# Performance work log

Measured on AMD Instinct MI355X. Metric: run time of the kernel, lower is better.

The kernel has to match this reference:

```python
import jax, jax.numpy as jnp
import numpy as np

B, T, C, H = 2, 2048, 768, 12
D = C // H              # head_dim = 64
LOCAL_WINDOW = 256
LN_EPS = 1e-5


def _layernorm(x, w, b):
    mu = jnp.mean(x, axis=-1, keepdims=True)
    var = jnp.var(x, axis=-1, keepdims=True)
    return (x - mu) * jax.lax.rsqrt(var + LN_EPS) * w + b


def setup_inputs() -> dict:
    key = jax.random.key(0)
    ks = jax.random.split(key, 8)
    inp = {
        "x": jax.random.normal(ks[0], (B, T, C), dtype=jnp.float32),
        "mamba_raw": jax.random.normal(ks[1], (B, T, C), dtype=jnp.float32),
        # c_attn / c_proj per nn.init in __init__
        "c_attn_w": 0.02 * jax.random.normal(ks[2], (C, 3 * C), dtype=jnp.float32),
        "c_attn_b": jnp.zeros((3 * C,), dtype=jnp.float32),
        "c_proj_w": 0.02 * jax.random.normal(ks[3], (C, C), dtype=jnp.float32),
        "c_proj_b": jnp.zeros((C,), dtype=jnp.float32),
        "ln_w": jnp.ones((C,), dtype=jnp.float32),
        "ln_b": jnp.zeros((C,), dtype=jnp.float32),
        "mamba_scale": jnp.asarray(0.1, dtype=jnp.float32),
        "sel_w": 0.01 * jax.random.normal(ks[4], (C, 1), dtype=jnp.float32),
        "sel_b": jnp.zeros((1,), dtype=jnp.float32),
        "local_weight": jnp.asarray(0.5, dtype=jnp.float32),
        "global_weight": jnp.asarray(0.5, dtype=jnp.float32),
    }
    return inp


def reference(x, mamba_raw, c_attn_w, c_attn_b, c_proj_w, c_proj_b,
              ln_w, ln_b, mamba_scale, sel_w, sel_b, local_weight, global_weight):
    scale = D ** -0.5
    qkv = x @ c_attn_w + c_attn_b                       # (B,T,3C)
    q, k, v = jnp.split(qkv, 3, axis=-1)
    q = q.reshape(B, T, H, D)
    k = k.reshape(B, T, H, D)
    v = v.reshape(B, T, H, D)

    scores = jnp.einsum('bihd,bjhd->bhij', q, k) * scale  # (B,H,T,T)
    i = jnp.arange(T)[:, None]
    j = jnp.arange(T)[None, :]
    causal = j > i                                       # mask strictly-future keys
    neg_inf = jnp.asarray(-jnp.inf, dtype=scores.dtype)
    scores = jnp.where(causal, neg_inf, scores)

    # frozen mamba branch (mamba_raw is a constant activation)
    mamba_raw = jax.lax.stop_gradient(mamba_raw)
    mamba_scaled = mamba_scale * _layernorm(mamba_raw, ln_w, ln_b)   # (B,T,C)
    sel = jax.nn.sigmoid(mamba_scaled @ sel_w + sel_b)               # (B,T,1)
    sel = sel[:, None, :, 0][:, :, None, :]                          # (B,1,1,T) over keys

    attn_global = scores * (0.5 + 0.5 * sel)             # -inf stays -inf

    outside_local = j < jnp.maximum(i - LOCAL_WINDOW, 0)
    attn_local = jnp.where(outside_local, neg_inf, scores)

    w_l = jax.nn.sigmoid(local_weight)
    w_g = jax.nn.sigmoid(global_weight)
    w_sum = w_l + w_g
    w_l, w_g = w_l / w_sum, w_g / w_sum

    attn_combined = w_l * jax.nn.softmax(attn_local, axis=-1) \
                  + w_g * jax.nn.softmax(attn_global, axis=-1)

    out = jnp.einsum('bhij,bjhd->bihd', attn_combined, v).reshape(B, T, C)
    return out @ c_proj_w + c_proj_b
```

## Files before the change

kernel.cpp:

```cpp
#include <hip/hip_runtime.h>
#include <math.h>

#define Bsz 2
#define Tsz 2048
#define Csz 768
#define Hsz 12
#define C3  2304
#define WIN 256
#define LN_EPS 1e-5f

#define QSCALE 0.1803368801111137f

typedef short bf16x8 __attribute__((ext_vector_type(8)));
typedef float f32x4  __attribute__((ext_vector_type(4)));

__device__ __forceinline__ unsigned short f2b(float f) {
    unsigned int u = __float_as_uint(f);
    u = (u + 0x7fffu + ((u >> 16) & 1u)) >> 16;
    return (unsigned short)u;
}

__device__ __forceinline__ float fast_exp2(float x) {
    float r;
    asm("v_exp_f32 %0, %1" : "=v"(r) : "v"(x));
    return r;
}

__global__ __launch_bounds__(256) void prep_fused(
    const float* __restrict__ x, unsigned short* __restrict__ xb,
    const float* __restrict__ c_attn_w, unsigned short* __restrict__ wq,
    const float* __restrict__ c_proj_w, unsigned short* __restrict__ wp,
    const float* __restrict__ mr, const float* __restrict__ ln_w,
    const float* __restrict__ ln_b, const float* __restrict__ scale_p,
    const float* __restrict__ sel_w, const float* __restrict__ sel_b,
    float* __restrict__ sel)
{
    __shared__ float tile[32][33];
    __shared__ float red1[256];
    __shared__ float red2[256];
    __shared__ float mu_sh, rstd_sh;

    const int blk = blockIdx.x;
    const int tid = threadIdx.x;

    if (blk < 3072) {
        int idx = blk * 256 + tid;
        float4 v = *(const float4*)(x + (size_t)idx * 4);
        unsigned int lo = (unsigned int)f2b(v.x) | ((unsigned int)f2b(v.y) << 16);
        unsigned int hi = (unsigned int)f2b(v.z) | ((unsigned int)f2b(v.w) << 16);
        uint2 o; o.x = lo; o.y = hi;
        *(uint2*)(xb + (size_t)idx * 4) = o;
        return;
    }
    if (blk < 5376) {
        const float* src; unsigned short* dst; int K, N, n0, k0;
        if (blk < 4800) {
            int i = blk - 3072;
            src = c_attn_w; dst = wq; K = Csz; N = C3;
            n0 = (i % 72) * 32; k0 = (i / 72) * 32;
        } else {
            int i = blk - 4800;
            src = c_proj_w; dst = wp; K = Csz; N = Csz;
            n0 = (i % 24) * 32; k0 = (i / 24) * 32;
        }
        const int tx = tid & 31, ty = tid >> 5;
        #pragma unroll
        for (int p = 0; p < 4; ++p)
            tile[ty + p * 8][tx] = src[(size_t)(k0 + ty + p * 8) * N + n0 + tx];
        __syncthreads();
        #pragma unroll
        for (int p = 0; p < 4; ++p)
            dst[(size_t)(n0 + ty + p * 8) * K + k0 + tx] = f2b(tile[tx][ty + p * 8]);
        return;
    }

    const int r = blk - 5376;
    const float* row = mr + (size_t)r * Csz;

    float s = 0.f, s2 = 0.f;
    for (int c = tid; c < Csz; c += 256) {
        float xv = row[c];
        s += xv; s2 += xv * xv;
    }
    red1[tid] = s; red2[tid] = s2;
    __syncthreads();
    for (int st = 128; st > 0; st >>= 1) {
        if (tid < st) { red1[tid] += red1[tid + st]; red2[tid] += red2[tid + st]; }
        __syncthreads();
    }
    if (tid == 0) {
        float mu = red1[0] * (1.f / Csz);
        float var = red2[0] * (1.f / Csz) - mu * mu;
        mu_sh = mu;
        rstd_sh = rsqrtf(var + LN_EPS);
    }
    __syncthreads();
    const float mu = mu_sh, rstd = rstd_sh;

    float dot = 0.f;
    for (int c = tid; c < Csz; c += 256) {
        float xn = (row[c] - mu) * rstd * ln_w[c] + ln_b[c];
        dot += xn * sel_w[c];
    }
    red1[tid] = dot;
    __syncthreads();
    for (int st = 128; st > 0; st >>= 1) {
        if (tid < st) red1[tid] += red1[tid + st];
        __syncthreads();
    }
    if (tid == 0) {
        float z = scale_p[0] * red1[0] + sel_b[0];
        sel[r] = 0.5f + 0.5f / (1.f + __expf(-z));
    }
}

__global__ __launch_bounds__(256) void pack_fused(
    const unsigned short* __restrict__ qkv, unsigned short* __restrict__ KP,
    unsigned short* __restrict__ VP)
{
    __shared__ unsigned short tile[32][72];

    if (blockIdx.x < 1536) {
        const int g = blockIdx.x * 4 + (threadIdx.x >> 6);
        const int lane = threadIdx.x & 63;
        const int lm = lane & 15, quad = lane >> 4;
        const int f = g & 1;
        const int kt = (g >> 1) & 127;
        const int bh = g >> 8;
        const int b = bh / Hsz, h = bh % Hsz;
        const unsigned short* src = qkv +
            (size_t)(b * Tsz + kt * 16 + lm) * C3 + Csz + h * 64 + f * 32 + quad * 8;
        bf16x8 v = *(const bf16x8*)src;
        *(bf16x8*)(KP + (size_t)g * 512 + lane * 8) = v;
        return;
    }

    const int g = blockIdx.x - 1536;
    const int jt = g & 63;
    const int bh = g >> 6;
    const int b = bh / Hsz, h = bh % Hsz;

    const int row = threadIdx.x >> 3, dc = (threadIdx.x & 7) * 8;
    *(bf16x8*)&tile[row][dc] = *(const bf16x8*)(
        qkv + (size_t)(b * Tsz + jt * 32 + row) * C3 + 2 * Csz + h * 64 + dc);
    __syncthreads();

    const int lane = threadIdx.x & 63, nt = threadIdx.x >> 6;
    const int lm = lane & 15, quad = lane >> 4;
    unsigned short tmp[8];
    #pragma unroll
    for (int j = 0; j < 8; ++j) tmp[j] = tile[quad * 8 + j][nt * 16 + lm];
    *(bf16x8*)(VP + ((size_t)(bh * 64 + jt) * 4 + nt) * 512 + lane * 8) =
        *(bf16x8*)tmp;
}

template<int OUT_BF16>
__global__ __launch_bounds__(256) void gemm_bt_mfma(
    const unsigned short* __restrict__ A, const unsigned short* __restrict__ BT,
    const float* __restrict__ bias, void* __restrict__ Cout,
    int M, int N, int K, int scale_cols)
{
    __shared__ unsigned short As[128 * 32];
    __shared__ unsigned short Bs[128 * 32];

    const int tid = threadIdx.x;
    const int lane = tid & 63, widx = tid >> 6;
    const int lm = lane & 15, quad = lane >> 4;
    const int wm = widx >> 1, wn = widx & 1;
    const int m0 = blockIdx.y * 128, n0 = blockIdx.x * 128;

    f32x4 acc[4][4];
    #pragma unroll
    for (int mt = 0; mt < 4; ++mt)
        #pragma unroll
        for (int nt = 0; nt < 4; ++nt)
            acc[mt][nt] = f32x4{0.f, 0.f, 0.f, 0.f};

    int rowS[2], cS[2];
    #pragma unroll
    for (int t = 0; t < 2; ++t) {
        int idx = t * 256 + tid;
        rowS[t] = idx >> 2;
        cS[t] = idx & 3;
    }

    bf16x8 pa[2], pb[2];
    #pragma unroll
    for (int t = 0; t < 2; ++t) {
        pa[t] = *(const bf16x8*)(A + (size_t)(m0 + rowS[t]) * K + cS[t] * 8);
        pb[t] = *(const bf16x8*)(BT + (size_t)(n0 + rowS[t]) * K + cS[t] * 8);
    }

    const int nk = K / 32;
    for (int kt = 0; kt < nk; ++kt) {
        __syncthreads();
        #pragma unroll
        for (int t = 0; t < 2; ++t) {
            *(bf16x8*)(&As[rowS[t] * 32 + ((cS[t] ^ ((rowS[t] >> 1) & 3)) << 3)]) = pa[t];
            *(bf16x8*)(&Bs[rowS[t] * 32 + ((cS[t] ^ ((rowS[t] >> 1) & 3)) << 3)]) = pb[t];
        }
        __syncthreads();
        if (kt + 1 < nk) {
            int k0 = (kt + 1) * 32;
            #pragma unroll
            for (int t = 0; t < 2; ++t) {
                pa[t] = *(const bf16x8*)(A + (size_t)(m0 + rowS[t]) * K + k0 + cS[t] * 8);
                pb[t] = *(const bf16x8*)(BT + (size_t)(n0 + rowS[t]) * K + k0 + cS[t] * 8);
            }
        }
        bf16x8 af[4], bf[4];
        #pragma unroll
        for (int mt = 0; mt < 4; ++mt) {
            int m = wm * 64 + mt * 16 + lm;
            af[mt] = *(const bf16x8*)(&As[m * 32 + ((quad ^ ((m >> 1) & 3)) << 3)]);
        }
        #pragma unroll
        for (int nt = 0; nt < 4; ++nt) {
            int n = wn * 64 + nt * 16 + lm;
            bf[nt] = *(const bf16x8*)(&Bs[n * 32 + ((quad ^ ((n >> 1) & 3)) << 3)]);
        }
        #pragma unroll
        for (int mt = 0; mt < 4; ++mt)
            #pragma unroll
            for (int nt = 0; nt < 4; ++nt)
                acc[mt][nt] = __builtin_amdgcn_mfma_f32_16x16x32_bf16(
                    af[mt], bf[nt], acc[mt][nt], 0, 0, 0);
    }

    float bv[4], scl[4];
    #pragma unroll
    for (int nt = 0; nt < 4; ++nt) {
        bv[nt] = bias[n0 + wn * 64 + nt * 16 + lm];
        scl[nt] = ((n0 + wn * 64 + nt * 16) < scale_cols) ? QSCALE : 1.0f;
    }

    #pragma unroll
    for (int mt = 0; mt < 4; ++mt) {
        #pragma unroll
        for (int nt = 0; nt < 4; ++nt) {
            int col = n0 + wn * 64 + nt * 16 + lm;
            #pragma unroll
            for (int r = 0; r < 4; ++r) {
                int row = m0 + wm * 64 + mt * 16 + quad * 4 + r;
                float v = (acc[mt][nt][r] + bv[nt]) * scl[nt];
                if (OUT_BF16)
                    ((unsigned short*)Cout)[(size_t)row * N + col] = f2b(v);
                else
                    ((float*)Cout)[(size_t)row * N + col] = v;
            }
        }
    }
}

__global__ __launch_bounds__(256) void attn_mfma(
    const unsigned short* __restrict__ qkv, const unsigned short* __restrict__ KP,
    const unsigned short* __restrict__ VP, const float* __restrict__ fsel_arr,
    const float* __restrict__ lw_p, const float* __restrict__ gw_p,
    unsigned short* __restrict__ attnb)
{
    __shared__ __align__(16) unsigned char SMEM[18432];

    const int tid = threadIdx.x;
    const int widx = tid >> 6, lane = tid & 63;
    const int lm = lane & 15, quad = lane >> 4;

    unsigned short* Pg = (unsigned short*)SMEM + (widx * 2 + 0) * (16 * 72);
    unsigned short* Pl = (unsigned short*)SMEM + (widx * 2 + 1) * (16 * 72);
    float* MrgF = (float*)SMEM;
    #define MRG(slot, br, row, col) MrgF[((((slot) * 2 + (br)) * 16 + (row)) * 66) + (col)]

    const int strip = 127 - (int)(blockIdx.x / 24);
    const int bh = (int)(blockIdx.x % 24);
    const int h = bh % Hsz, b = bh / Hsz;
    const int i0 = strip * 16;

    const unsigned short* qkv_b = qkv + (size_t)b * Tsz * C3;
    const unsigned short* KPb = KP + (size_t)bh * 131072 + lane * 8;
    const unsigned short* VPb = VP + (size_t)bh * 131072 + lane * 8;

    const unsigned short* qrow = qkv_b + (size_t)(i0 + lm) * C3 + h * 64 + quad * 8;
    const bf16x8 qf0 = *(const bf16x8*)qrow;
    const bf16x8 qf1 = *(const bf16x8*)(qrow + 32);

    float l_g[4], l_l[4];
    f32x4 Og[4], Ol[4];
    #pragma unroll
    for (int r = 0; r < 4; ++r) { l_g[r] = 0.f; l_l[r] = 0.f; }
    #pragma unroll
    for (int nt = 0; nt < 4; ++nt) {
        Og[nt] = f32x4{0.f, 0.f, 0.f, 0.f};
        Ol[nt] = f32x4{0.f, 0.f, 0.f, 0.f};
    }

    const int jtd = i0 >> 6;
    const int jtl = (jtd - 4) > 0 ? (jtd - 4) : 0;

    for (int jt = widx; jt <= jtd; jt += 4) {
        const int j0 = jt * 64;
        const bool diag = (jt == jtd);
        const bool firstloc = (jt == jtl) && !diag;
        const bool loc = (jt >= jtl);

        const unsigned short* kp = KPb + (size_t)(j0 >> 4) * 1024;
        bf16x8 kc0[4], kc1[4];
        #pragma unroll
        for (int nt = 0; nt < 4; ++nt) {
            kc0[nt] = *(const bf16x8*)(kp + nt * 1024);
            kc1[nt] = *(const bf16x8*)(kp + nt * 1024 + 512);
        }

        f32x4 s[4];
        #pragma unroll
        for (int nt = 0; nt < 4; ++nt) {
            f32x4 z = f32x4{0.f, 0.f, 0.f, 0.f};
            z = __builtin_amdgcn_mfma_f32_16x16x32_bf16(qf0, kc0[nt], z, 0, 0, 0);
            z = __builtin_amdgcn_mfma_f32_16x16x32_bf16(qf1, kc1[nt], z, 0, 0, 0);
            s[nt] = z;
        }

        float fs[4];
        #pragma unroll
        for (int nt = 0; nt < 4; ++nt)
            fs[nt] = fsel_arr[b * Tsz + j0 + nt * 16 + lm];

        if (diag) {
            #pragma unroll
            for (int r = 0; r < 4; ++r) {
                const int qi = i0 + quad * 4 + r;
                #pragma unroll
                for (int nt = 0; nt < 4; ++nt) {
                    const int kj = j0 + nt * 16 + lm;
                    float p = fast_exp2(s[nt][r] * fs[nt]);
                    p = (kj > qi) ? 0.f : p;
                    unsigned int u = __float_as_uint(p);
                    l_g[r] += __uint_as_float(u & 0xffff0000u);
                    Pg[(quad * 4 + r) * 72 + nt * 16 + lm] = (unsigned short)(u >> 16);
                }
            }
        } else {
            #pragma unroll
            for (int r = 0; r < 4; ++r)
                #pragma unroll
                for (int nt = 0; nt < 4; ++nt) {
                    float p = fast_exp2(s[nt][r] * fs[nt]);
                    unsigned int u = __float_as_uint(p);
                    l_g[r] += __uint_as_float(u & 0xffff0000u);
                    Pg[(quad * 4 + r) * 72 + nt * 16 + lm] = (unsigned short)(u >> 16);
                }
        }

        if (loc) {
            if (diag) {
                #pragma unroll
                for (int r = 0; r < 4; ++r) {
                    const int qi = i0 + quad * 4 + r;
                    #pragma unroll
                    for (int nt = 0; nt < 4; ++nt) {
                        const int kj = j0 + nt * 16 + lm;
                        float p = fast_exp2(s[nt][r]);
                        p = (kj > qi || kj < qi - WIN) ? 0.f : p;
                        unsigned int u = __float_as_uint(p);
                        l_l[r] += __uint_as_float(u & 0xffff0000u);
                        Pl[(quad * 4 + r) * 72 + nt * 16 + lm] = (unsigned short)(u >> 16);
                    }
                }
            } else if (firstloc) {
                #pragma unroll
                for (int r = 0; r < 4; ++r) {
                    const int qi = i0 + quad * 4 + r;
                    #pragma unroll
                    for (int nt = 0; nt < 4; ++nt) {
                        const int kj = j0 + nt * 16 + lm;
                        float p = fast_exp2(s[nt][r]);
                        p = (kj < qi - WIN) ? 0.f : p;
                        unsigned int u = __float_as_uint(p);
                        l_l[r] += __uint_as_float(u & 0xffff0000u);
                        Pl[(quad * 4 + r) * 72 + nt * 16 + lm] = (unsigned short)(u >> 16);
                    }
                }
            } else {
                #pragma unroll
                for (int r = 0; r < 4; ++r)
                    #pragma unroll
                    for (int nt = 0; nt < 4; ++nt) {
                        float p = fast_exp2(s[nt][r]);
                        unsigned int u = __float_as_uint(p);
                        l_l[r] += __uint_as_float(u & 0xffff0000u);
                        Pl[(quad * 4 + r) * 72 + nt * 16 + lm] = (unsigned short)(u >> 16);
                    }
            }
        }

        const bf16x8 ag0 = *(const bf16x8*)(&Pg[lm * 72 + quad * 8]);
        const bf16x8 ag1 = *(const bf16x8*)(&Pg[lm * 72 + 32 + quad * 8]);
        bf16x8 al0 = {}, al1 = {};
        if (loc) {
            al0 = *(const bf16x8*)(&Pl[lm * 72 + quad * 8]);
            al1 = *(const bf16x8*)(&Pl[lm * 72 + 32 + quad * 8]);
        }

        const unsigned short* vp = VPb + (size_t)(j0 >> 5) * 2048;
        #pragma unroll
        for (int nt = 0; nt < 4; ++nt) {
            bf16x8 v0 = *(const bf16x8*)(vp + nt * 512);
            bf16x8 v1 = *(const bf16x8*)(vp + 2048 + nt * 512);
            Og[nt] = __builtin_amdgcn_mfma_f32_16x16x32_bf16(ag0, v0, Og[nt], 0, 0, 0);
            Og[nt] = __builtin_amdgcn_mfma_f32_16x16x32_bf16(ag1, v1, Og[nt], 0, 0, 0);
            if (loc) {
                Ol[nt] = __builtin_amdgcn_mfma_f32_16x16x32_bf16(al0, v0, Ol[nt], 0, 0, 0);
                Ol[nt] = __builtin_amdgcn_mfma_f32_16x16x32_bf16(al1, v1, Ol[nt], 0, 0, 0);
            }
        }
    }

    #pragma unroll
    for (int st = 1; st < 16; st <<= 1) {
        #pragma unroll
        for (int r = 0; r < 4; ++r) {
            l_g[r] += __shfl_xor(l_g[r], st);
            l_l[r] += __shfl_xor(l_l[r], st);
        }
    }

    auto write_slot = [&](int slot) {
        #pragma unroll
        for (int r = 0; r < 4; ++r) {
            const int row = quad * 4 + r;
            #pragma unroll
            for (int nt = 0; nt < 4; ++nt) {
                MRG(slot, 0, row, nt * 16 + lm) = Og[nt][r];
                MRG(slot, 1, row, nt * 16 + lm) = Ol[nt][r];
            }
            if (lm == 0) {
                MRG(slot, 0, row, 65) = l_g[r];
                MRG(slot, 1, row, 65) = l_l[r];
            }
        }
    };
    auto combine_slot = [&](int slot) {
        #pragma unroll
        for (int r = 0; r < 4; ++r) {
            const int row = quad * 4 + r;
            {
                l_g[r] += MRG(slot, 0, row, 65);
                #pragma unroll
                for (int nt = 0; nt < 4; ++nt)
                    Og[nt][r] += MRG(slot, 0, row, nt * 16 + lm);
            }
            {
                l_l[r] += MRG(slot, 1, row, 65);
                #pragma unroll
                for (int nt = 0; nt < 4; ++nt)
                    Ol[nt][r] += MRG(slot, 1, row, nt * 16 + lm);
            }
        }
    };

    __syncthreads();
    if (widx == 1) write_slot(0);
    if (widx == 3) write_slot(1);
    __syncthreads();
    if (widx == 0) combine_slot(0);
    if (widx == 2) combine_slot(1);
    __syncthreads();
    if (widx == 2) write_slot(0);
    __syncthreads();

    if (widx == 0) {
        combine_slot(0);

        float wl = 1.f / (1.f + __expf(-lw_p[0]));
        float wg = 1.f / (1.f + __expf(-gw_p[0]));
        float ws = wl + wg;
        wl /= ws; wg /= ws;

        #pragma unroll
        for (int r = 0; r < 4; ++r) {
            const int row = quad * 4 + r;
            const float cg = wg / l_g[r];
            const float cl = wl / l_l[r];
            #pragma unroll
            for (int nt = 0; nt < 4; ++nt) {
                float v = Og[nt][r] * cg + Ol[nt][r] * cl;
                attnb[(size_t)(b * Tsz + i0 + row) * Csz + h * 64 + nt * 16 + lm] =
                    f2b(v);
            }
        }
    }
    #undef MRG
}

extern "C" void kernel_launch(void* const* d_in, const int* in_sizes, int n_in,
                              void* d_out, int out_size, void* d_ws, size_t ws_size,
                              hipStream_t stream)
{
    const float* x          = (const float*)d_in[0];
    const float* mamba_raw  = (const float*)d_in[1];
    const float* c_attn_w   = (const float*)d_in[2];
    const float* c_attn_b   = (const float*)d_in[3];
    const float* c_proj_w   = (const float*)d_in[4];
    const float* c_proj_b   = (const float*)d_in[5];
    const float* ln_w       = (const float*)d_in[6];
    const float* ln_b       = (const float*)d_in[7];
    const float* mamba_sc   = (const float*)d_in[8];
    const float* sel_w      = (const float*)d_in[9];
    const float* sel_b      = (const float*)d_in[10];
    const float* local_w    = (const float*)d_in[11];
    const float* global_w   = (const float*)d_in[12];
    float* out = (float*)d_out;

    const int M = Bsz * Tsz;

    unsigned short* xb    = (unsigned short*)d_ws;
    unsigned short* wq    = xb + (size_t)M * Csz;
    unsigned short* wp    = wq + (size_t)C3 * Csz;
    unsigned short* qkvb  = wp + (size_t)Csz * Csz;
    unsigned short* kpb   = qkvb + (size_t)M * C3;
    unsigned short* vpb   = kpb + (size_t)24 * 131072;
    unsigned short* attnb = vpb + (size_t)24 * 131072;
    float* sel = (float*)(attnb + (size_t)M * Csz);

    prep_fused<<<9472, 256, 0, stream>>>(x, xb, c_attn_w, wq, c_proj_w, wp,
                                         mamba_raw, ln_w, ln_b, mamba_sc,
                                         sel_w, sel_b, sel);

    {
        dim3 g(C3 / 128, M / 128);
        gemm_bt_mfma<1><<<g, 256, 0, stream>>>(xb, wq, c_attn_b, qkvb,
                                               M, C3, Csz, Csz);
    }

    pack_fused<<<3072, 256, 0, stream>>>(qkvb, kpb, vpb);

    attn_mfma<<<128 * Hsz * Bsz, 256, 0, stream>>>(qkvb, kpb, vpb, sel,
                                                   local_w, global_w, attnb);

    {
        dim3 g(Csz / 128, M / 128);
        gemm_bt_mfma<0><<<g, 256, 0, stream>>>(attnb, wp, c_proj_b, out,
                                               M, Csz, Csz, 0);
    }
}
```

Measured before the change: 198.0 us.

## Fuse K/V packing into QKV GEMM epilogue and double-buffer attention tiles

The QKV projection GEMM now writes Q to a compact buffer and scatters K and V straight into the MFMA-friendly packed layouts, so the separate pack kernel and the full qkv intermediate are gone. The attention loop processes two key tiles per iteration: it runs the score and softmax phase for both before their PV phases, using doubled shared memory for the P buffers to expose more independent work. The trade-offs are scattered 2-byte global stores in the GEMM epilogue and twice the LDS per block, which may lower occupancy.

New measurement: 193.9 us. 2.1% less time.

```diff
diff --git a/kernel.cpp b/kernel.cpp
--- a/kernel.cpp
+++ b/kernel.cpp
@@ -114,51 +114,12 @@
     }
 }
 
-__global__ __launch_bounds__(256) void pack_fused(
-    const unsigned short* __restrict__ qkv, unsigned short* __restrict__ KP,
-    unsigned short* __restrict__ VP)
-{
-    __shared__ unsigned short tile[32][72];
-
-    if (blockIdx.x < 1536) {
-        const int g = blockIdx.x * 4 + (threadIdx.x >> 6);
-        const int lane = threadIdx.x & 63;
-        const int lm = lane & 15, quad = lane >> 4;
-        const int f = g & 1;
-        const int kt = (g >> 1) & 127;
-        const int bh = g >> 8;
-        const int b = bh / Hsz, h = bh % Hsz;
-        const unsigned short* src = qkv +
-            (size_t)(b * Tsz + kt * 16 + lm) * C3 + Csz + h * 64 + f * 32 + quad * 8;
-        bf16x8 v = *(const bf16x8*)src;
-        *(bf16x8*)(KP + (size_t)g * 512 + lane * 8) = v;
-        return;
-    }
-
-    const int g = blockIdx.x - 1536;
-    const int jt = g & 63;
-    const int bh = g >> 6;
-    const int b = bh / Hsz, h = bh % Hsz;
-
-    const int row = threadIdx.x >> 3, dc = (threadIdx.x & 7) * 8;
-    *(bf16x8*)&tile[row][dc] = *(const bf16x8*)(
-        qkv + (size_t)(b * Tsz + jt * 32 + row) * C3 + 2 * Csz + h * 64 + dc);
-    __syncthreads();
-
-    const int lane = threadIdx.x & 63, nt = threadIdx.x >> 6;
-    const int lm = lane & 15, quad = lane >> 4;
-    unsigned short tmp[8];
-    #pragma unroll
-    for (int j = 0; j < 8; ++j) tmp[j] = tile[quad * 8 + j][nt * 16 + lm];
-    *(bf16x8*)(VP + ((size_t)(bh * 64 + jt) * 4 + nt) * 512 + lane * 8) =
-        *(bf16x8*)tmp;
-}
-
-template<int OUT_BF16>
+template<int MODE>
 __global__ __launch_bounds__(256) void gemm_bt_mfma(
     const unsigned short* __restrict__ A, const unsigned short* __restrict__ BT,
     const float* __restrict__ bias, void* __restrict__ Cout,
-    int M, int N, int K, int scale_cols)
+    unsigned short* __restrict__ KP, unsigned short* __restrict__ VP,
+    int M, int N, int K)
 {
     __shared__ unsigned short As[128 * 32];
     __shared__ unsigned short Bs[128 * 32];
@@ -227,45 +188,72 @@
                     af[mt], bf[nt], acc[mt][nt], 0, 0, 0);
     }
 
-    float bv[4], scl[4];
-    #pragma unroll
-    for (int nt = 0; nt < 4; ++nt) {
+    float bv[4];
+    #pragma unroll
+    for (int nt = 0; nt < 4; ++nt)
         bv[nt] = bias[n0 + wn * 64 + nt * 16 + lm];
-        scl[nt] = ((n0 + wn * 64 + nt * 16) < scale_cols) ? QSCALE : 1.0f;
-    }
 
     #pragma unroll
     for (int mt = 0; mt < 4; ++mt) {
         #pragma unroll
         for (int nt = 0; nt < 4; ++nt) {
-            int col = n0 + wn * 64 + nt * 16 + lm;
-            #pragma unroll
-            for (int r = 0; r < 4; ++r) {
-                int row = m0 + wm * 64 + mt * 16 + quad * 4 + r;
-                float v = (acc[mt][nt][r] + bv[nt]) * scl[nt];
-                if (OUT_BF16)
-                    ((unsigned short*)Cout)[(size_t)row * N + col] = f2b(v);
-                else
-                    ((float*)Cout)[(size_t)row * N + col] = v;
+            const int cb = n0 + wn * 64 + nt * 16;
+            const int col = cb + lm;
+            const int rbase = m0 + wm * 64 + mt * 16 + quad * 4;
+            if (MODE == 0) {
+                #pragma unroll
+                for (int r = 0; r < 4; ++r)
+                    ((float*)Cout)[(size_t)(rbase + r) * N + col] =
+                        acc[mt][nt][r] + bv[nt];
+            } else if (cb < Csz) {
+                #pragma unroll
+                for (int r = 0; r < 4; ++r)
+                    ((unsigned short*)Cout)[(size_t)(rbase + r) * Csz + col] =
+                        f2b((acc[mt][nt][r] + bv[nt]) * QSCALE);
+            } else if (cb < 2 * Csz) {
+                const int dfull = col - Csz;
+                const int h = dfull >> 6, dd = dfull & 63;
+                const int f = dd >> 5, qd = (dd >> 3) & 3, j = dd & 7;
+                #pragma unroll
+                for (int r = 0; r < 4; ++r) {
+                    const int row = rbase + r;
+                    const int b = row >> 11, t = row & 2047;
+                    const int ktk = t >> 4, lmk = t & 15;
+                    size_t addr = ((((size_t)((b * Hsz + h) * 128 + ktk)) * 2 + f) * 512)
+                                  + (qd * 16 + lmk) * 8 + j;
+                    KP[addr] = f2b(acc[mt][nt][r] + bv[nt]);
+                }
+            } else {
+                const int dfull = col - 2 * Csz;
+                const int h = dfull >> 6, dd = dfull & 63;
+                const int ntv = dd >> 4, lmv = dd & 15;
+                #pragma unroll
+                for (int r = 0; r < 4; ++r) {
+                    const int row = rbase + r;
+                    const int b = row >> 11, t = row & 2047;
+                    const int jtv = t >> 5, qv = (t >> 3) & 3, j = t & 7;
+                    size_t addr = (((size_t)((b * Hsz + h) * 64 + jtv) * 4 + ntv) * 512)
+                                  + (qv * 16 + lmv) * 8 + j;
+                    VP[addr] = f2b(acc[mt][nt][r] + bv[nt]);
+                }
             }
         }
     }
 }
 
 __global__ __launch_bounds__(256) void attn_mfma(
-    const unsigned short* __restrict__ qkv, const unsigned short* __restrict__ KP,
+    const unsigned short* __restrict__ qb, const unsigned short* __restrict__ KP,
     const unsigned short* __restrict__ VP, const float* __restrict__ fsel_arr,
     const float* __restrict__ lw_p, const float* __restrict__ gw_p,
     unsigned short* __restrict__ attnb)
 {
-    __shared__ __align__(16) unsigned char SMEM[18432];
+    __shared__ __align__(16) unsigned char SMEM[36864];
 
     const int tid = threadIdx.x;
     const int widx = tid >> 6, lane = tid & 63;
     const int lm = lane & 15, quad = lane >> 4;
 
-    unsigned short* Pg = (unsigned short*)SMEM + (widx * 2 + 0) * (16 * 72);
-    unsigned short* Pl = (unsigned short*)SMEM + (widx * 2 + 1) * (16 * 72);
+    unsigned short* Pb = (unsigned short*)SMEM + widx * 4 * (16 * 72);
     float* MrgF = (float*)SMEM;
     #define MRG(slot, br, row, col) MrgF[((((slot) * 2 + (br)) * 16 + (row)) * 66) + (col)]
 
@@ -274,11 +262,11 @@
     const int h = bh % Hsz, b = bh / Hsz;
     const int i0 = strip * 16;
 
-    const unsigned short* qkv_b = qkv + (size_t)b * Tsz * C3;
     const unsigned short* KPb = KP + (size_t)bh * 131072 + lane * 8;
     const unsigned short* VPb = VP + (size_t)bh * 131072 + lane * 8;
 
-    const unsigned short* qrow = qkv_b + (size_t)(i0 + lm) * C3 + h * 64 + quad * 8;
+    const unsigned short* qrow =
+        qb + (size_t)(b * Tsz + i0 + lm) * Csz + h * 64 + quad * 8;
     const bf16x8 qf0 = *(const bf16x8*)qrow;
     const bf16x8 qf1 = *(const bf16x8*)(qrow + 32);
 
@@ -295,26 +283,23 @@
     const int jtd = i0 >> 6;
     const int jtl = (jtd - 4) > 0 ? (jtd - 4) : 0;
 
-    for (int jt = widx; jt <= jtd; jt += 4) {
+    auto phaseA = [&](int jt, int slot) {
         const int j0 = jt * 64;
         const bool diag = (jt == jtd);
         const bool firstloc = (jt == jtl) && !diag;
         const bool loc = (jt >= jtl);
+        unsigned short* Pg = Pb + (slot * 2 + 0) * (16 * 72);
+        unsigned short* Pl = Pb + (slot * 2 + 1) * (16 * 72);
 
         const unsigned short* kp = KPb + (size_t)(j0 >> 4) * 1024;
-        bf16x8 kc0[4], kc1[4];
+        f32x4 s[4];
         #pragma unroll
         for (int nt = 0; nt < 4; ++nt) {
-            kc0[nt] = *(const bf16x8*)(kp + nt * 1024);
-            kc1[nt] = *(const bf16x8*)(kp + nt * 1024 + 512);
-        }
-
-        f32x4 s[4];
-        #pragma unroll
-        for (int nt = 0; nt < 4; ++nt) {
+            bf16x8 k0 = *(const bf16x8*)(kp + nt * 1024);
+            bf16x8 k1 = *(const bf16x8*)(kp + nt * 1024 + 512);
             f32x4 z = f32x4{0.f, 0.f, 0.f, 0.f};
-            z = __builtin_amdgcn_mfma_f32_16x16x32_bf16(qf0, kc0[nt], z, 0, 0, 0);
-            z = __builtin_amdgcn_mfma_f32_16x16x32_bf16(qf1, kc1[nt], z, 0, 0, 0);
+            z = __builtin_amdgcn_mfma_f32_16x16x32_bf16(qf0, k0, z, 0, 0, 0);
+            z = __builtin_amdgcn_mfma_f32_16x16x32_bf16(qf1, k1, z, 0, 0, 0);
             s[nt] = z;
         }
 
@@ -390,6 +375,13 @@
                     }
             }
         }
+    };
+
+    auto phaseB = [&](int jt, int slot) {
+        const int j0 = jt * 64;
+        const bool loc = (jt >= jtl);
+        unsigned short* Pg = Pb + (slot * 2 + 0) * (16 * 72);
+        unsigned short* Pl = Pb + (slot * 2 + 1) * (16 * 72);
 
         const bf16x8 ag0 = *(const bf16x8*)(&Pg[lm * 72 + quad * 8]);
         const bf16x8 ag1 = *(const bf16x8*)(&Pg[lm * 72 + 32 + quad * 8]);
@@ -411,6 +403,15 @@
                 Ol[nt] = __builtin_amdgcn_mfma_f32_16x16x32_bf16(al1, v1, Ol[nt], 0, 0, 0);
             }
         }
+    };
+
+    for (int jt = widx; jt <= jtd; jt += 8) {
+        const int jt2 = jt + 4;
+        const bool has2 = (jt2 <= jtd);
+        phaseA(jt, 0);
+        if (has2) phaseA(jt2, 1);
+        phaseB(jt, 0);
+        if (has2) phaseB(jt2, 1);
     }
 
     #pragma unroll
@@ -514,8 +515,8 @@
     unsigned short* xb    = (unsigned short*)d_ws;
     unsigned short* wq    = xb + (size_t)M * Csz;
     unsigned short* wp    = wq + (size_t)C3 * Csz;
-    unsigned short* qkvb  = wp + (size_t)Csz * Csz;
-    unsigned short* kpb   = qkvb + (size_t)M * C3;
+    unsigned short* qb    = wp + (size_t)Csz * Csz;
+    unsigned short* kpb   = qb + (size_t)M * Csz;
     unsigned short* vpb   = kpb + (size_t)24 * 131072;
     unsigned short* attnb = vpb + (size_t)24 * 131072;
     float* sel = (float*)(attnb + (size_t)M * Csz);
@@ -526,18 +527,16 @@
 
     {
         dim3 g(C3 / 128, M / 128);
-        gemm_bt_mfma<1><<<g, 256, 0, stream>>>(xb, wq, c_attn_b, qkvb,
-                                               M, C3, Csz, Csz);
-    }
-
-    pack_fused<<<3072, 256, 0, stream>>>(qkvb, kpb, vpb);
-
-    attn_mfma<<<128 * Hsz * Bsz, 256, 0, stream>>>(qkvb, kpb, vpb, sel,
+        gemm_bt_mfma<1><<<g, 256, 0, stream>>>(xb, wq, c_attn_b, qb,
+                                               kpb, vpb, M, C3, Csz);
+    }
+
+    attn_mfma<<<128 * Hsz * Bsz, 256, 0, stream>>>(qb, kpb, vpb, sel,
                                                    local_w, global_w, attnb);
 
     {
         dim3 g(Csz / 128, M / 128);
         gemm_bt_mfma<0><<<g, 256, 0, stream>>>(attnb, wp, c_proj_b, out,
-                                               M, Csz, Csz, 0);
+                                               nullptr, nullptr, M, Csz, Csz);
     }
 }
```
